# Kernel optimization log

Measured on AMD Instinct MI355X. Metric: run time of the kernel, lower is better.

The kernel has to match this reference:

```python
import jax, jax.numpy as jnp
import numpy as np

B, C, E, K, Hh, Ww = 4, 64, 4, 5, 96, 96


def setup_inputs() -> dict:
    key = jax.random.key(0)
    ks = jax.random.split(key, 18)
    c8 = C // 8
    rn = lambda k, shape, s=0.05: jax.random.normal(k, shape, dtype=jnp.float32) * s
    return {
        "x": rn(ks[0], (B, C, Hh, Ww), 1.0),
        "st_feat": rn(ks[1], (B, C, Hh, Ww), 1.0),
        "kc_w": rn(ks[2], (C * K * K, C)), "kc_b": rn(ks[3], (C * K * K,)),
        "wc": rn(ks[4], (E, c8, C)), "we": rn(ks[5], (E, C, c8)),
        "body1_w": rn(ks[6], (64, 4)), "body1_b": rn(ks[7], (64,)),
        "body2_w": rn(ks[8], (64, 64)), "body2_b": rn(ks[9], (64,)),
        "rout_w": rn(ks[10], (E, 64)), "rout_b": rn(ks[11], (E,)),
        "off_w": rn(ks[12], (2, 64)), "off_b": rn(ks[13], (2,)),
        "stoff_w": rn(ks[14], (2, 64)), "stoff_b": rn(ks[15], (2,)),
        "fus_w": rn(ks[16], (C, 2 * C)), "fus_b": rn(ks[17], (C,)),
        "scale": 2,
    }


def _conv1x1(x, w, b):
    return jnp.einsum('oi,bihw->bohw', w, x) + b[None, :, None, None]


def _sta_conv(feat, kernel, k):
    # spatially-varying depthwise kxk conv: kernel [b, c*k*k, h, w], channel-major (ch*k*k + kh*k + kw)
    b, c, h, w = feat.shape
    pad = (k - 1) // 2
    fp = jnp.pad(feat, ((0, 0), (0, 0), (pad, pad), (pad, pad)), mode='edge')  # replicate pad
    patches = jnp.stack([fp[:, :, i:i + h, j:j + w] for i in range(k) for j in range(k)], axis=2)  # [b,c,k*k,h,w]
    kern = kernel.reshape(b, c, k * k, h, w)
    return jnp.sum(patches * kern, axis=2)


def _grid_sample(img, offset, sh, sw, H, W):
    # bilinear, zero padding, align_corners=True; offset [1or b, 2, H, W] in source-pixel units
    b, c, h, w = img.shape
    gx = ((jnp.arange(W, dtype=jnp.float32) + 0.5) / sw - 0.5) * 2.0 / (w - 1) - 1.0
    gy = ((jnp.arange(H, dtype=jnp.float32) + 0.5) / sh - 0.5) * 2.0 / (h - 1) - 1.0
    gx = jnp.broadcast_to(gx[None, None, :] + offset[:, 0] * 2.0 / (w - 1), (b, H, W))
    gy = jnp.broadcast_to(gy[None, :, None] + offset[:, 1] * 2.0 / (h - 1), (b, H, W))
    px = (gx + 1.0) * 0.5 * (w - 1)
    py = (gy + 1.0) * 0.5 * (h - 1)
    x0 = jnp.floor(px)
    y0 = jnp.floor(py)
    imgf = img.reshape(b, c, h * w)

    def gather(ix, iy):
        valid = (ix >= 0) & (ix <= w - 1) & (iy >= 0) & (iy <= h - 1)
        ixc = jnp.clip(ix, 0, w - 1).astype(jnp.int32)
        iyc = jnp.clip(iy, 0, h - 1).astype(jnp.int32)
        idx = (iyc * w + ixc).reshape(b, 1, H * W)
        v = jnp.take_along_axis(imgf, idx, axis=2).reshape(b, c, H, W)
        return v * valid.astype(img.dtype)[:, None]

    wx1 = (px - x0)[:, None]
    wy1 = (py - y0)[:, None]
    wx0 = 1.0 - wx1
    wy0 = 1.0 - wy1
    return (wy0 * wx0 * gather(x0, y0) + wy0 * wx1 * gather(x0 + 1.0, y0)
            + wy1 * wx0 * gather(x0, y0 + 1.0) + wy1 * wx1 * gather(x0 + 1.0, y0 + 1.0))


def _forward(x, st_feat, kc_w, kc_b, wc, we, body1_w, body1_b, body2_w, body2_b,
             rout_w, rout_b, off_w, off_b, stoff_w, stoff_b, fus_w, fus_b, scale):
    b, c, h, w = x.shape
    sh = sw = float(scale)
    H, W = int(h * sh), int(w * sw)
    c8 = c // 8
    num_e = wc.shape[0]

    kernel_warp = jax.nn.leaky_relu(_conv1x1(st_feat, kc_w, kc_b), 0.1)  # [b, c*K*K, h, w]
    sta_feat = _sta_conv(x, kernel_warp, K)

    # coordinate embedding input [1, 4, H, W]
    ch = (jnp.arange(H, dtype=jnp.float32) + 0.5) / sh
    coor_h = ch - jnp.floor(ch + 0.001) - 0.5  # [H]
    cw = (jnp.arange(W, dtype=jnp.float32) + 0.5) / sw
    coor_w = cw - jnp.floor(cw + 0.001) - 0.5  # [W]
    ones = jnp.ones((H, W), dtype=jnp.float32)
    inp = jnp.stack([ones / sw, ones / sh,
                     jnp.broadcast_to(coor_h[:, None], (H, W)),
                     jnp.broadcast_to(coor_w[None, :], (H, W))], axis=0)[None]

    emb = jax.nn.relu(_conv1x1(jax.nn.relu(_conv1x1(inp, body1_w, body1_b)), body2_w, body2_b))
    offset = _conv1x1(emb, off_w, off_b)       # [1, 2, H, W]
    st_offset = _conv1x1(emb, stoff_w, stoff_b)
    routing = jax.nn.sigmoid(_conv1x1(emb, rout_w, rout_b))  # [1, E, H, W]

    r = routing[0].reshape(num_e, H * W).T  # [HW, E]
    wc_px = (r @ wc.reshape(num_e, -1)).reshape(H, W, c8, c)
    we_px = (r @ we.reshape(num_e, -1)).reshape(H, W, c, c8)

    fea0 = _grid_sample(x, offset, sh, sw, H, W)  # [b, c, H, W]
    t = jnp.einsum('hwoc,bchw->bhwo', wc_px, fea0)
    fea = jnp.einsum('hwco,bhwo->bchw', we_px, t) + fea0

    sta_hr = _grid_sample(sta_feat, st_offset, sh, sw, H, W)
    out = _conv1x1(jnp.concatenate([sta_hr, fea], axis=1), fus_w, fus_b)
    return out


def reference(x, st_feat, kc_w, kc_b, wc, we, body1_w, body1_b, body2_w, body2_b,
              rout_w, rout_b, off_w, off_b, stoff_w, stoff_b, fus_w, fus_b, scale):
    return _forward(x, st_feat, kc_w, kc_b, wc, we, body1_w, body1_b, body2_w, body2_b,
                    rout_w, rout_b, off_w, off_b, stoff_w, stoff_b, fus_w, fus_b, scale)
```

## Files before the change

kernel.cpp:

```cpp
#include <hip/hip_runtime.h>

typedef __attribute__((ext_vector_type(8))) _Float16 h8;
typedef __attribute__((ext_vector_type(4))) _Float16 h4;
typedef __attribute__((ext_vector_type(4))) float f32x4;

__device__ __forceinline__ _Float16 f2h(float f) { return (_Float16)f; }
__device__ __forceinline__ float h2f(_Float16 h) { return (float)h; }

__device__ __forceinline__ int fswz(int p, int i) { return p * 128 + (i ^ ((p & 7) << 3)); }

#define WS_STA   0u
#define WS_GSI   4718592u
#define WS_GSF   4718656u
#define WS_WCPX  4718720u
#define WS_WEPX  4726912u
#define WS_FUSB  4735104u
#define WS_KCB   4751488u
#define WS_KCW   4757888u

__global__ __launch_bounds__(256) void k_prep(
    const float* __restrict__ kc_w, const float* __restrict__ kc_b,
    const float* __restrict__ fusw,
    _Float16* __restrict__ kcw, _Float16* __restrict__ fusB,
    float* __restrict__ kcbp)
{
  int e = blockIdx.x * 256 + threadIdx.x;
  if (e < 25600) {
    int jp = e >> 4, i0 = (e & 15) << 2;
    int w = jp / 400, rem = jp % 400;
    int t = rem >> 4, cl = rem & 15;
    int j = (w * 16 + cl) * 25 + t;
    const float4* src = (const float4*)(kc_w + j * 64 + i0);
    float4 v = *src;
    h4 ov;
    ov[0] = f2h(v.x); ov[1] = f2h(v.y); ov[2] = f2h(v.z); ov[3] = f2h(v.w);
    *(h4*)(kcw + jp * 64 + i0) = ov;
  }
  if (e < 8192) {
    int Nt = e >> 11, ks = (e >> 9) & 3, l = (e >> 3) & 63, j = e & 7;
    fusB[e] = f2h(fusw[(Nt * 16 + (l & 15)) * 128 + (l >> 4) * 8 + 32 * ks + j]);
  }
  if (e < 1600) {
    int w = e / 400, rem = e % 400, t = rem >> 4, cl = rem & 15;
    kcbp[e] = kc_b[(w * 16 + cl) * 25 + t];
  }
}

__global__ __launch_bounds__(256) void k_embed(
    const float* __restrict__ b1w, const float* __restrict__ b1b,
    const float* __restrict__ b2w, const float* __restrict__ b2b,
    const float* __restrict__ rw,  const float* __restrict__ rb,
    const float* __restrict__ ow,  const float* __restrict__ ob,
    const float* __restrict__ sow, const float* __restrict__ sob,
    const float* __restrict__ wc,  const float* __restrict__ we,
    int* __restrict__ gs_i, float* __restrict__ gs_f,
    float* __restrict__ wcpx, float* __restrict__ wepx)
{
  __shared__ float l_w2[4096];
  __shared__ float l_h1[4][64];
  __shared__ float l_h2[4][64];
  __shared__ float l_sm[4][8];
  int tid = threadIdx.x;
  for (int e = tid; e < 4096; e += 256) l_w2[e] = b2w[e];
  int g = tid >> 6, o = tid & 63;
  float py = (g >> 1) ? 1.f : 0.f;
  float pxx = (g & 1) ? 1.f : 0.f;
  float chh = (py + 0.5f) * 0.5f;
  float coh = chh - floorf(chh + 0.001f) - 0.5f;
  float cww = (pxx + 0.5f) * 0.5f;
  float cow = cww - floorf(cww + 0.001f) - 0.5f;
  float z = b1b[o] + b1w[o * 4 + 0] * 0.5f + b1w[o * 4 + 1] * 0.5f
          + b1w[o * 4 + 2] * coh + b1w[o * 4 + 3] * cow;
  l_h1[g][o] = fmaxf(z, 0.f);
  __syncthreads();
  float z2 = b2b[o];
  #pragma unroll 8
  for (int i = 0; i < 64; i++) z2 = fmaf(l_w2[o * 64 + i], l_h1[g][i], z2);
  l_h2[g][o] = fmaxf(z2, 0.f);
  __syncthreads();
  if (o < 8) {
    const float* wp; float bias;
    if (o < 4)      { wp = rw  + o * 64;       bias = rb[o]; }
    else if (o < 6) { wp = ow  + (o - 4) * 64; bias = ob[o - 4]; }
    else            { wp = sow + (o - 6) * 64; bias = sob[o - 6]; }
    float acc = bias;
    for (int i = 0; i < 64; i++) acc = fmaf(wp[i], l_h2[g][i], acc);
    if (o < 4) acc = 1.f / (1.f + expf(-acc));
    l_sm[g][o] = acc;
  }
  __syncthreads();
  if (o == 0) {
    float qbx = (g & 1) ? 0.25f : -0.25f;
    float qby = (g >> 1) ? 0.25f : -0.25f;
    float qx  = qbx + l_sm[g][4]; float fx  = floorf(qx);
    float qy  = qby + l_sm[g][5]; float fy  = floorf(qy);
    float qsx = qbx + l_sm[g][6]; float fsx = floorf(qsx);
    float qsy = qby + l_sm[g][7]; float fsy = floorf(qsy);
    gs_i[g * 4 + 0] = (int)fx;  gs_f[g * 4 + 0] = qx - fx;
    gs_i[g * 4 + 1] = (int)fy;  gs_f[g * 4 + 1] = qy - fy;
    gs_i[g * 4 + 2] = (int)fsx; gs_f[g * 4 + 2] = qsx - fsx;
    gs_i[g * 4 + 3] = (int)fsy; gs_f[g * 4 + 3] = qsy - fsy;
  }
  float r0 = l_sm[g][0], r1 = l_sm[g][1], r2 = l_sm[g][2], r3 = l_sm[g][3];
  for (int idx = o; idx < 512; idx += 64) {
    wcpx[g * 512 + idx] = r0 * wc[idx] + r1 * wc[512 + idx] + r2 * wc[1024 + idx] + r3 * wc[1536 + idx];
    wepx[g * 512 + idx] = r0 * we[idx] + r1 * we[512 + idx] + r2 * we[1024 + idx] + r3 * we[1536 + idx];
  }
}

__global__ __launch_bounds__(512, 4) void k_sta(
    const float* __restrict__ x, const float* __restrict__ st,
    const _Float16* __restrict__ kcw, const float* __restrict__ kcbp,
    _Float16* __restrict__ sta_out)
{
  __shared__ __align__(16) _Float16 x_lds[64 * 5 * 40];
  __shared__ __align__(16) _Float16 st_lds[32 * 72];
  int wg = (blockIdx.x & 7) * 144 + (blockIdx.x >> 3);
  int b = wg / 288;
  int r1 = wg % 288;
  int hb = r1 / 3, wb = r1 % 3;
  int tid = threadIdx.x, lane = tid & 63;
  int w = (tid >> 6) & 3, half = tid >> 8;
  for (int e = tid; e < 2560; e += 512) {
    int row = e >> 3, v = e & 7;
    int rr = row % 5;
    int grow = min(max(hb + rr - 2, 0), 95);
    float4 val = *(const float4*)&x[((b * 64 + (row / 5)) * 96 + grow) * 96 + 32 * wb + v * 4];
    _Float16* dst = &x_lds[row * 40 + 2 + v * 4];
    dst[0] = f2h(val.x); dst[1] = f2h(val.y); dst[2] = f2h(val.z); dst[3] = f2h(val.w);
  }
  for (int e = tid; e < 1280; e += 512) {
    int row = e >> 2, j = e & 3;
    int col = (j < 2) ? j : 32 + j;
    int rr = row % 5;
    int grow = min(max(hb + rr - 2, 0), 95);
    int gcol = min(max(32 * wb + col - 2, 0), 95);
    x_lds[row * 40 + col] = f2h(x[((b * 64 + (row / 5)) * 96 + grow) * 96 + gcol]);
  }
  for (int e = tid; e < 512; e += 512) {
    int c = e >> 3, p0 = (e & 7) * 4;
    float4 v = *(const float4*)&st[((size_t)(b * 64 + c) * 96 + hb) * 96 + 32 * wb + p0];
    st_lds[(p0 + 0) * 72 + c] = f2h(v.x);
    st_lds[(p0 + 1) * 72 + c] = f2h(v.y);
    st_lds[(p0 + 2) * 72 + c] = f2h(v.z);
    st_lds[(p0 + 3) * 72 + c] = f2h(v.w);
  }
  __syncthreads();
  int l15 = lane & 15, lg = lane >> 4;
  h8 afrag[2];
  #pragma unroll
  for (int ks = 0; ks < 2; ks++)
    afrag[ks] = *(const h8*)&st_lds[(half * 16 + l15) * 72 + 32 * ks + lg * 8];
  float sta_acc[4];
  #pragma unroll
  for (int r = 0; r < 4; r++) sta_acc[r] = 0.f;
  for (int dh = 0; dh < 5; dh++) {
    const _Float16* xp = &x_lds[((w * 16 + l15) * 5 + dh) * 40 + half * 16 + lg * 4];
    h4 xa0 = *(const h4*)xp;
    h4 xa1 = *(const h4*)(xp + 4);
    float kb5[5];
    #pragma unroll
    for (int dw = 0; dw < 5; dw++)
      kb5[dw] = kcbp[w * 400 + (dh * 5 + dw) * 16 + l15];
    #pragma unroll
    for (int dw = 0; dw < 5; dw++) {
      int jbase = w * 400 + (dh * 5 + dw) * 16;
      const _Float16* bp = kcw + (jbase + l15) * 64 + lg * 8;
      h8 bf0 = *(const h8*)bp;
      h8 bf1 = *(const h8*)(bp + 32);
      f32x4 acc = {0.f, 0.f, 0.f, 0.f};
      acc = __builtin_amdgcn_mfma_f32_16x16x32_f16(afrag[0], bf0, acc, 0, 0, 0);
      acc = __builtin_amdgcn_mfma_f32_16x16x32_f16(afrag[1], bf1, acc, 0, 0, 0);
      #pragma unroll
      for (int r = 0; r < 4; r++) {
        float kw = acc[r] + kb5[dw];
        kw = (kw >= 0.f) ? kw : 0.1f * kw;
        int ci = r + dw;
        float xvf = h2f(ci < 4 ? xa0[ci] : xa1[ci - 4]);
        sta_acc[r] = fmaf(kw, xvf, sta_acc[r]);
      }
    }
  }
  {
    h4 ov;
    #pragma unroll
    for (int r = 0; r < 4; r++) ov[r] = f2h(sta_acc[r]);
    _Float16* tp = sta_out + ((size_t)((b * 96 + hb) * 3 + wb) << 11);
    *(h4*)(tp + (w * 16 + l15) * 32 + half * 16 + lg * 4) = ov;
  }
}

__global__ __launch_bounds__(256) void k_main(
    const float* __restrict__ x, const _Float16* __restrict__ sta,
    const int* __restrict__ gs_i, const float* __restrict__ gs_f,
    const float* __restrict__ wcpx, const float* __restrict__ wepx,
    const _Float16* __restrict__ fusB, const float* __restrict__ fusb,
    float* __restrict__ out)
{
  __shared__ __align__(16) _Float16 feat[64 * 128];
  __shared__ float t_lds[8][68];
  int wg = (blockIdx.x & 7) * 288 + (blockIdx.x >> 3);
  int b = wg / 576, r = wg % 576;
  int y = r / 3, xb = r % 3;
  int tid = threadIdx.x, px = tid & 63, fg = tid >> 6;
  int xg = xb * 64 + px;
  int v = ((y & 1) << 1) | (xg & 1);
  int idxo = gs_i[v * 4 + 0], idyo = gs_i[v * 4 + 1], idxs = gs_i[v * 4 + 2], idys = gs_i[v * 4 + 3];
  float wx1 = gs_f[v * 4 + 0], wy1 = gs_f[v * 4 + 1], sx1 = gs_f[v * 4 + 2], sy1 = gs_f[v * 4 + 3];
  int xh = xg >> 1, yh = y >> 1;
  int ix0 = xh + idxo, iy0 = yh + idyo;
  float wx0 = 1.f - wx1, wy0 = 1.f - wy1;
  bool vx0 = (unsigned)ix0 < 96u, vx1 = (unsigned)(ix0 + 1) < 96u;
  bool vy0 = (unsigned)iy0 < 96u, vy1 = (unsigned)(iy0 + 1) < 96u;
  int cx0 = min(max(ix0, 0), 95), cx1 = min(max(ix0 + 1, 0), 95);
  int cy0 = min(max(iy0, 0), 95), cy1 = min(max(iy0 + 1, 0), 95);
  float ww00 = (vx0 && vy0) ? wy0 * wx0 : 0.f;
  float ww10 = (vx1 && vy0) ? wy0 * wx1 : 0.f;
  float ww01 = (vx0 && vy1) ? wy1 * wx0 : 0.f;
  float ww11 = (vx1 && vy1) ? wy1 * wx1 : 0.f;
  int a00 = cy0 * 96 + cx0, a10 = cy0 * 96 + cx1, a01 = cy1 * 96 + cx0, a11 = cy1 * 96 + cx1;
  int jx0 = xh + idxs, jy0 = yh + idys;
  float sx0 = 1.f - sx1, sy0 = 1.f - sy1;
  bool ux0 = (unsigned)jx0 < 96u, ux1 = (unsigned)(jx0 + 1) < 96u;
  bool uy0 = (unsigned)jy0 < 96u, uy1 = (unsigned)(jy0 + 1) < 96u;
  int dx0 = min(max(jx0, 0), 95), dx1 = min(max(jx0 + 1, 0), 95);
  int dy0 = min(max(jy0, 0), 95), dy1 = min(max(jy0 + 1, 0), 95);
  float sw00 = (ux0 && uy0) ? sy0 * sx0 : 0.f;
  float sw10 = (ux1 && uy0) ? sy0 * sx1 : 0.f;
  float sw01 = (ux0 && uy1) ? sy1 * sx0 : 0.f;
  float sw11 = (ux1 && uy1) ? sy1 * sx1 : 0.f;
  int s00 = (((b * 96 + dy0) * 3 + (dx0 >> 5)) << 11) + (dx0 & 31);
  int s10 = (((b * 96 + dy0) * 3 + (dx1 >> 5)) << 11) + (dx1 & 31);
  int s01 = (((b * 96 + dy1) * 3 + (dx0 >> 5)) << 11) + (dx0 & 31);
  int s11 = (((b * 96 + dy1) * 3 + (dx1 >> 5)) << 11) + (dx1 & 31);
  h8 stv0, stv1, fev0, fev1;
  #pragma unroll
  for (int k = 0; k < 16; k++) {
    int ch = fg * 16 + k;
    const float* xc = x + (size_t)(b * 64 + ch) * 9216;
    float f0 = ww00 * xc[a00] + ww10 * xc[a10] + ww01 * xc[a01] + ww11 * xc[a11];
    const _Float16* sc = sta + ch * 32;
    float s0 = sw00 * h2f(sc[s00]) + sw10 * h2f(sc[s10]) + sw01 * h2f(sc[s01]) + sw11 * h2f(sc[s11]);
    if (k < 8) { stv0[k] = f2h(s0); fev0[k] = f2h(f0); }
    else       { stv1[k - 8] = f2h(s0); fev1[k - 8] = f2h(f0); }
  }
  *(h8*)&feat[fswz(px, fg * 16)]          = stv0;
  *(h8*)&feat[fswz(px, fg * 16 + 8)]      = stv1;
  *(h8*)&feat[fswz(px, 64 + fg * 16)]     = fev0;
  *(h8*)&feat[fswz(px, 64 + fg * 16 + 8)] = fev1;
  __syncthreads();
  {
    int o2 = fg * 2;
    int v0 = (y & 1) << 1;
    int base = __builtin_amdgcn_readfirstlane((v0 * 8 + o2) * 64);
    const float* w00 = wcpx + base;
    const float* w01 = wcpx + base + 64;
    const float* w10 = wcpx + base + 512;
    const float* w11 = wcpx + base + 512 + 64;
    float acc00 = 0.f, acc01 = 0.f, acc10 = 0.f, acc11 = 0.f;
    #pragma unroll
    for (int cb = 0; cb < 8; cb++) {
      h8 blk = *(const h8*)&feat[fswz(px, 64 + cb * 8)];
      #pragma unroll
      for (int q = 0; q < 8; q++) {
        float fv = h2f(blk[q]);
        int c = cb * 8 + q;
        acc00 = fmaf(w00[c], fv, acc00);
        acc01 = fmaf(w01[c], fv, acc01);
        acc10 = fmaf(w10[c], fv, acc10);
        acc11 = fmaf(w11[c], fv, acc11);
      }
    }
    bool odd = (xg & 1);
    t_lds[o2][px]     = odd ? acc10 : acc00;
    t_lds[o2 + 1][px] = odd ? acc11 : acc01;
  }
  __syncthreads();
  {
    float tv[8];
    #pragma unroll
    for (int oo = 0; oo < 8; oo++) tv[oo] = t_lds[oo][px];
    int v0 = (y & 1) << 1;
    bool odd = (xg & 1);
    int wbase = __builtin_amdgcn_readfirstlane((v0 * 64 + fg * 16) * 8);
    #pragma unroll
    for (int blki = 0; blki < 2; blki++) {
      h8 f0b = *(const h8*)&feat[fswz(px, 64 + fg * 16 + blki * 8)];
      h8 ob2;
      #pragma unroll
      for (int q = 0; q < 8; q++) {
        int k = blki * 8 + q;
        const float* wA = wepx + wbase + k * 8;
        const float* wB = wA + 512;
        float sA = 0.f, sB = 0.f;
        #pragma unroll
        for (int oo = 0; oo < 8; oo++) { sA = fmaf(wA[oo], tv[oo], sA); sB = fmaf(wB[oo], tv[oo], sB); }
        float fe = h2f(f0b[q]) + (odd ? sB : sA);
        ob2[q] = f2h(fe);
      }
      *(h8*)&feat[fswz(px, 64 + fg * 16 + blki * 8)] = ob2;
    }
  }
  __syncthreads();
  {
    int l15 = px & 15, lg = px >> 4;
    h8 af[4];
    #pragma unroll
    for (int ks = 0; ks < 4; ks++)
      af[ks] = *(const h8*)&feat[fswz(fg * 16 + l15, lg * 8 + 32 * ks)];
    #pragma unroll
    for (int Nt = 0; Nt < 4; Nt++) {
      f32x4 acc = {0.f, 0.f, 0.f, 0.f};
      #pragma unroll
      for (int ks = 0; ks < 4; ks++) {
        h8 bfv = *(const h8*)&fusB[((Nt * 4 + ks) * 64 + px) * 8];
        acc = __builtin_amdgcn_mfma_f32_16x16x32_f16(af[ks], bfv, acc, 0, 0, 0);
      }
      int c = Nt * 16 + l15;
      float bias = fusb[c];
      float4 o4;
      o4.x = acc[0] + bias; o4.y = acc[1] + bias; o4.z = acc[2] + bias; o4.w = acc[3] + bias;
      float* op = out + ((size_t)(b * 64 + c) * 192 + y) * 192 + xb * 64 + fg * 16 + lg * 4;
      *(float4*)op = o4;
    }
  }
}

extern "C" void kernel_launch(void* const* d_in, const int* in_sizes, int n_in,
                              void* d_out, int out_size, void* d_ws, size_t ws_size,
                              hipStream_t stream)
{
  (void)in_sizes; (void)n_in; (void)out_size; (void)ws_size;
  const float* x    = (const float*)d_in[0];
  const float* st   = (const float*)d_in[1];
  const float* kc_w = (const float*)d_in[2];
  const float* kc_b = (const float*)d_in[3];
  const float* wc   = (const float*)d_in[4];
  const float* we   = (const float*)d_in[5];
  const float* b1w  = (const float*)d_in[6];
  const float* b1b  = (const float*)d_in[7];
  const float* b2w  = (const float*)d_in[8];
  const float* b2b  = (const float*)d_in[9];
  const float* rw   = (const float*)d_in[10];
  const float* rb   = (const float*)d_in[11];
  const float* ow   = (const float*)d_in[12];
  const float* ob   = (const float*)d_in[13];
  const float* sow  = (const float*)d_in[14];
  const float* sob  = (const float*)d_in[15];
  const float* fusw = (const float*)d_in[16];
  const float* fusb = (const float*)d_in[17];
  char* ws = (char*)d_ws;
  _Float16* sta  = (_Float16*)(ws + WS_STA);
  int*   gsi  = (int*)(ws + WS_GSI);
  float* gsf  = (float*)(ws + WS_GSF);
  float* wcpxp = (float*)(ws + WS_WCPX);
  float* wepxp = (float*)(ws + WS_WEPX);
  _Float16* fusB = (_Float16*)(ws + WS_FUSB);
  float* kcbp = (float*)(ws + WS_KCB);
  _Float16* kcw = (_Float16*)(ws + WS_KCW);
  float* outp = (float*)d_out;

  k_prep<<<dim3(100), dim3(256), 0, stream>>>(kc_w, kc_b, fusw, kcw, fusB, kcbp);
  k_embed<<<dim3(1), dim3(256), 0, stream>>>(b1w, b1b, b2w, b2b, rw, rb, ow, ob,
                                             sow, sob, wc, we, gsi, gsf, wcpxp, wepxp);
  k_sta<<<dim3(1152), dim3(512), 0, stream>>>(x, st, kcw, kcbp, sta);
  k_main<<<dim3(2304), dim3(256), 0, stream>>>(x, sta, gsi, gsf, wcpxp, wepxp, fusB, fusb, outp);
}
```

Before: 208.6 us.

## Stage predicted-kernel weights in LDS per row, prelaid in MFMA fragment order

```diff
diff --git a/kernel.cpp b/kernel.cpp
--- a/kernel.cpp
+++ b/kernel.cpp
@@ -21,20 +21,19 @@
 __global__ __launch_bounds__(256) void k_prep(
     const float* __restrict__ kc_w, const float* __restrict__ kc_b,
     const float* __restrict__ fusw,
-    _Float16* __restrict__ kcw, _Float16* __restrict__ fusB,
+    _Float16* __restrict__ kcw2, _Float16* __restrict__ fusB,
     float* __restrict__ kcbp)
 {
   int e = blockIdx.x * 256 + threadIdx.x;
-  if (e < 25600) {
-    int jp = e >> 4, i0 = (e & 15) << 2;
-    int w = jp / 400, rem = jp % 400;
-    int t = rem >> 4, cl = rem & 15;
-    int j = (w * 16 + cl) * 25 + t;
-    const float4* src = (const float4*)(kc_w + j * 64 + i0);
-    float4 v = *src;
-    h4 ov;
-    ov[0] = f2h(v.x); ov[1] = f2h(v.y); ov[2] = f2h(v.z); ov[3] = f2h(v.w);
-    *(h4*)(kcw + jp * 64 + i0) = ov;
+  if (e < 12800) {
+    int h = e & 1, lane = (e >> 1) & 63, w = (e >> 7) & 3, tap = e >> 9;
+    int l15 = lane & 15, lg = lane >> 4;
+    int j = (w * 16 + l15) * 25 + tap;
+    const float* s = kc_w + j * 64 + h * 32 + lg * 8;
+    h8 ov;
+    #pragma unroll
+    for (int q = 0; q < 8; q++) ov[q] = f2h(s[q]);
+    *(h8*)(kcw2 + ((tap * 4 + w) * 2 + h) * 512 + lane * 8) = ov;
   }
   if (e < 8192) {
     int Nt = e >> 11, ks = (e >> 9) & 3, l = (e >> 3) & 63, j = e & 7;
@@ -110,11 +109,13 @@
 
 __global__ __launch_bounds__(512, 4) void k_sta(
     const float* __restrict__ x, const float* __restrict__ st,
-    const _Float16* __restrict__ kcw, const float* __restrict__ kcbp,
+    const _Float16* __restrict__ kcw2, const float* __restrict__ kcbp,
     _Float16* __restrict__ sta_out)
 {
   __shared__ __align__(16) _Float16 x_lds[64 * 5 * 40];
   __shared__ __align__(16) _Float16 st_lds[32 * 72];
+  __shared__ __align__(16) _Float16 kw_lds[20480];
+  __shared__ float bias_lds[1600];
   int wg = (blockIdx.x & 7) * 144 + (blockIdx.x >> 3);
   int b = wg / 288;
   int r1 = wg % 288;
@@ -137,14 +138,15 @@
     int gcol = min(max(32 * wb + col - 2, 0), 95);
     x_lds[row * 40 + col] = f2h(x[((b * 64 + (row / 5)) * 96 + grow) * 96 + gcol]);
   }
-  for (int e = tid; e < 512; e += 512) {
-    int c = e >> 3, p0 = (e & 7) * 4;
+  if (tid < 512) {
+    int c = tid >> 3, p0 = (tid & 7) * 4;
     float4 v = *(const float4*)&st[((size_t)(b * 64 + c) * 96 + hb) * 96 + 32 * wb + p0];
     st_lds[(p0 + 0) * 72 + c] = f2h(v.x);
     st_lds[(p0 + 1) * 72 + c] = f2h(v.y);
     st_lds[(p0 + 2) * 72 + c] = f2h(v.z);
     st_lds[(p0 + 3) * 72 + c] = f2h(v.w);
   }
+  if (tid < 400) *(float4*)&bias_lds[tid * 4] = *(const float4*)&kcbp[tid * 4];
   __syncthreads();
   int l15 = lane & 15, lg = lane >> 4;
   h8 afrag[2];
@@ -155,19 +157,26 @@
   #pragma unroll
   for (int r = 0; r < 4; r++) sta_acc[r] = 0.f;
   for (int dh = 0; dh < 5; dh++) {
+    if (dh) __syncthreads();
+    {
+      const uint4* src = (const uint4*)((const char*)kcw2 + dh * 40960);
+      uint4* dst = (uint4*)kw_lds;
+      #pragma unroll
+      for (int s = 0; s < 5; s++)
+        dst[s * 512 + tid] = src[s * 512 + tid];
+    }
+    __syncthreads();
     const _Float16* xp = &x_lds[((w * 16 + l15) * 5 + dh) * 40 + half * 16 + lg * 4];
     h4 xa0 = *(const h4*)xp;
     h4 xa1 = *(const h4*)(xp + 4);
     float kb5[5];
     #pragma unroll
     for (int dw = 0; dw < 5; dw++)
-      kb5[dw] = kcbp[w * 400 + (dh * 5 + dw) * 16 + l15];
+      kb5[dw] = bias_lds[w * 400 + (dh * 5 + dw) * 16 + l15];
     #pragma unroll
     for (int dw = 0; dw < 5; dw++) {
-      int jbase = w * 400 + (dh * 5 + dw) * 16;
-      const _Float16* bp = kcw + (jbase + l15) * 64 + lg * 8;
-      h8 bf0 = *(const h8*)bp;
-      h8 bf1 = *(const h8*)(bp + 32);
+      h8 bf0 = *(const h8*)&kw_lds[(dw * 4 + w) * 1024 + lane * 8];
+      h8 bf1 = *(const h8*)&kw_lds[(dw * 4 + w) * 1024 + 512 + lane * 8];
       f32x4 acc = {0.f, 0.f, 0.f, 0.f};
       acc = __builtin_amdgcn_mfma_f32_16x16x32_f16(afrag[0], bf0, acc, 0, 0, 0);
       acc = __builtin_amdgcn_mfma_f32_16x16x32_f16(afrag[1], bf1, acc, 0, 0, 0);
@@ -357,12 +366,12 @@
   float* wepxp = (float*)(ws + WS_WEPX);
   _Float16* fusB = (_Float16*)(ws + WS_FUSB);
   float* kcbp = (float*)(ws + WS_KCB);
-  _Float16* kcw = (_Float16*)(ws + WS_KCW);
+  _Float16* kcw2 = (_Float16*)(ws + WS_KCW);
   float* outp = (float*)d_out;
 
-  k_prep<<<dim3(100), dim3(256), 0, stream>>>(kc_w, kc_b, fusw, kcw, fusB, kcbp);
+  k_prep<<<dim3(100), dim3(256), 0, stream>>>(kc_w, kc_b, fusw, kcw2, fusB, kcbp);
   k_embed<<<dim3(1), dim3(256), 0, stream>>>(b1w, b1b, b2w, b2b, rw, rb, ow, ob,
                                              sow, sob, wc, we, gsi, gsf, wcpxp, wepxp);
-  k_sta<<<dim3(1152), dim3(512), 0, stream>>>(x, st, kcw, kcbp, sta);
+  k_sta<<<dim3(1152), dim3(512), 0, stream>>>(x, st, kcw2, kcbp, sta);
   k_main<<<dim3(2304), dim3(256), 0, stream>>>(x, sta, gsi, gsf, wcpxp, wepxp, fusB, fusb, outp);
 }
```

New measurement: 198.0 us. -5.1%, faster.
